# Kernel optimization log

Measured on AMD Instinct MI355X. Metric: run time of the kernel, lower is better.

Reference implementation:

```python
import jax, jax.numpy as jnp
import numpy as np
from jax import lax


def setup_inputs() -> dict:
    key = jax.random.key(0)
    ks = jax.random.split(key, 16)
    B, H, W, C = 4, 48, 48, 512
    N = H * W
    std = 0.02  # trunc_normal std in the torch init

    def nrm(k, shape, s=std):
        return jax.random.normal(k, shape, dtype=jnp.float32) * s

    return {
        "x": jax.random.normal(ks[0], (B, N, C), jnp.float32),
        "context": jax.random.normal(ks[1], (B, N, C), jnp.float32),
        "mask1": jax.random.uniform(ks[2], (B, N), jnp.float32),
        "mask2": jax.random.uniform(ks[3], (B, N), jnp.float32),
        "q_w": nrm(ks[4], (C, C)), "q_b": jnp.zeros((C,), jnp.float32),
        "kv1_w": nrm(ks[5], (C, C)), "kv1_b": jnp.zeros((C,), jnp.float32),
        "kv2_w": nrm(ks[6], (C, C)), "kv2_b": jnp.zeros((C,), jnp.float32),
        "f1_w": nrm(ks[7], (1, 48)), "f1_b": jnp.zeros((1,), jnp.float32),
        "f2_w": nrm(ks[8], (1, 12)), "f2_b": jnp.zeros((1,), jnp.float32),
        "lepe_w": nrm(ks[9], (C, C)), "lepe_b": jnp.zeros((C,), jnp.float32),
        "lepe_conv_w": nrm(ks[10], (C, 1, 3, 3), float(np.sqrt(2.0 / 9.0))),
        "lepe_conv_b": jnp.zeros((C,), jnp.float32),
        "proj_w": nrm(ks[11], (C, C)), "proj_b": jnp.zeros((C,), jnp.float32),
        "H": H, "W": W,
    }


def _lin(t, w, b):
    # torch nn.Linear: y = t @ W^T + b, W:[out,in]
    return t @ w.T + b


def _pooled_seq(ctx, idx, f1_w, f1_b, f2_w, f2_b):
    # ctx:[B,HW,C], idx:[B,HW] mask-sorted indices. sr_ratio==4 => groups of 48/12/1.
    B, HW, Cc = ctx.shape
    t1, t2 = HW // 192, HW // 24  # token1=(HW//48)//4, token2=(HW//12)//2
    g = jnp.take_along_axis(ctx, idx[:, :, None], axis=1)  # [B,HW,C] gathered
    p1 = g[:, : HW // 4].transpose(0, 2, 1).reshape(B, Cc, t1, 48)
    p2 = g[:, HW // 4 : 3 * HW // 4].transpose(0, 2, 1).reshape(B, Cc, t2, 12)
    p3 = g[:, 3 * HW // 4 :].transpose(0, 2, 1)  # [B,C,HW//4]
    a1 = (p1 @ f1_w.T)[..., 0] + f1_b  # [B,C,t1]
    a2 = (p2 @ f2_w.T)[..., 0] + f2_b  # [B,C,t2]
    return jnp.concatenate([a1, a2, p3], axis=-1).transpose(0, 2, 1)  # [B,Lkv,C]


def reference(x, context, mask1, mask2, q_w, q_b, kv1_w, kv1_b, kv2_w, kv2_b,
              f1_w, f1_b, f2_w, f2_b, lepe_w, lepe_b, lepe_conv_w, lepe_conv_b,
              proj_w, proj_b, H, W):
    B, N, C = x.shape
    nh = 8
    hd = C // nh
    scale = hd ** -0.5

    # lepe: linear + depthwise 3x3 conv positional encoding
    le = _lin(x, lepe_w, lepe_b).transpose(0, 2, 1).reshape(B, C, H, W)
    le = lax.conv_general_dilated(le, lepe_conv_w, (1, 1), ((1, 1), (1, 1)),
                                  dimension_numbers=("NCHW", "OIHW", "NCHW"),
                                  feature_group_count=C)
    lepe = (le + lepe_conv_b[None, :, None, None]).reshape(B, C, N).transpose(0, 2, 1)

    # mask-sorted grouped pooling of context (two orderings: row-major and transposed)
    idx1 = jnp.argsort(mask1, axis=1)
    idx2 = jnp.argsort(mask2, axis=1)
    ctx_t = context.reshape(B, H, W, C).transpose(0, 2, 1, 3).reshape(B, N, C)
    seq1 = _pooled_seq(context, idx1, f1_w, f1_b, f2_w, f2_b)
    seq2 = _pooled_seq(ctx_t, idx2, f1_w, f1_b, f2_w, f2_b)

    q = _lin(x, q_w, q_b).reshape(B, N, nh, hd).transpose(0, 2, 1, 3)  # [B,h,N,hd]
    kv1 = _lin(seq1, kv1_w, kv1_b).reshape(B, -1, 2, nh // 2, hd).transpose(2, 0, 3, 1, 4)
    kv2 = _lin(seq2, kv2_w, kv2_b).reshape(B, -1, 2, nh // 2, hd).transpose(2, 0, 3, 1, 4)
    k = jnp.concatenate([kv1[0], kv2[0]], axis=1)  # [B,h,Lkv,hd]
    v = jnp.concatenate([kv1[1], kv2[1]], axis=1)

    attn = jax.nn.softmax(jnp.einsum("bhnd,bhld->bhnl", q, k) * scale, axis=-1)
    out = jnp.einsum("bhnl,bhld->bhnd", attn, v).transpose(0, 2, 1, 3).reshape(B, N, C)
    return _lin(out + lepe, proj_w, proj_b)
```

## Files before the change

kernel.cpp:

```cpp
#include <hip/hip_runtime.h>
#include <hip/hip_bf16.h>
#include <math.h>

#define B_    4
#define H_    48
#define W_    48
#define N_    2304
#define C_    512
#define NH_   8
#define HD_   64
#define LKV_  684
#define LKP_  704

typedef __attribute__((ext_vector_type(8))) short short8;
typedef __attribute__((ext_vector_type(8))) unsigned short ushort8;
typedef __attribute__((ext_vector_type(4))) float f32x4;

#define MFMA16(a, b, c) __builtin_amdgcn_mfma_f32_16x16x32_bf16(a, b, c, 0, 0, 0)

__device__ __forceinline__ unsigned short f2bf(float f) {
  __hip_bfloat16 h = __float2bfloat16(f);
  return *reinterpret_cast<unsigned short*>(&h);
}
__device__ __forceinline__ float bf2f(unsigned short u) {
  unsigned int x = ((unsigned int)u) << 16;
  return *reinterpret_cast<float*>(&x);
}
__device__ __forceinline__ void gld16(const unsigned short* g, unsigned short* l) {
  __builtin_amdgcn_global_load_lds(
      (const __attribute__((address_space(1))) void*)g,
      (__attribute__((address_space(3))) void*)l, 16, 0, 0);
}

__global__ __launch_bounds__(256) void pack_all(
    const float* __restrict__ lepe_w, const float* __restrict__ q_w,
    const float* __restrict__ kv1_w, const float* __restrict__ kv2_w,
    const float* __restrict__ proj_w, const float* __restrict__ x,
    unsigned short* __restrict__ wb, unsigned short* __restrict__ xb)
{
  int i = (blockIdx.x * 256 + threadIdx.x) * 4;
  const float* s; unsigned short* d; int rel;
  if      (i < 262144)  { s = lepe_w; d = wb;           rel = i; }
  else if (i < 524288)  { s = q_w;    d = wb + 262144;  rel = i - 262144; }
  else if (i < 786432)  { s = kv1_w;  d = wb + 524288;  rel = i - 524288; }
  else if (i < 1048576) { s = kv2_w;  d = wb + 786432;  rel = i - 786432; }
  else if (i < 1310720) { s = proj_w; d = wb + 1048576; rel = i - 1048576; }
  else                  { s = x;      d = xb;           rel = i - 1310720; }
  float4 v = *(const float4*)(s + rel);
  ushort4 o;
  o.x = f2bf(v.x); o.y = f2bf(v.y); o.z = f2bf(v.z); o.w = f2bf(v.w);
  *(ushort4*)(d + rel) = o;
}

struct GPair {
  const unsigned short *A0, *A1, *B0, *B1;
  const float *bias0, *bias1;
  void *out0, *out1;
  int bf0, bf1;
  float sc0, sc1;
};

__global__ __launch_bounds__(256) void gemm_bf16(GPair p, int K, int Nn)
{
  const unsigned short* A  = blockIdx.z ? p.A1 : p.A0;
  const unsigned short* Bw = blockIdx.z ? p.B1 : p.B0;
  const float* bias        = blockIdx.z ? p.bias1 : p.bias0;
  void* out                = blockIdx.z ? p.out1 : p.out0;
  const int out_bf16       = blockIdx.z ? p.bf1 : p.bf0;
  const float oscale       = blockIdx.z ? p.sc1 : p.sc0;

  __shared__ unsigned short Abuf[128 * 32];
  __shared__ unsigned short Bbuf[128 * 32];
  const int tid = threadIdx.x;
  const int l = tid & 63, w = tid >> 6;
  const int wm = w >> 1, wn = w & 1;
  const int lo16 = l & 15, hi = l >> 4;
  const int row0 = blockIdx.x * 128, col0 = blockIdx.y * 128;
  const int srow = tid >> 2, scol = (tid & 3) * 8;

  const unsigned short* Asrc = A + (size_t)(row0 + srow) * K + scol;
  const unsigned short* Bsrc = Bw + (size_t)(col0 + srow) * K + scol;

  f32x4 acc[4][4];
  #pragma unroll
  for (int m = 0; m < 4; ++m)
    #pragma unroll
    for (int n = 0; n < 4; ++n)
      #pragma unroll
      for (int r = 0; r < 4; ++r) acc[m][n][r] = 0.f;

  for (int k0 = 0; k0 < K; k0 += 32) {
    __syncthreads();
    gld16(Asrc + k0,                   &Abuf[tid * 8]);
    gld16(Asrc + (size_t)64 * K + k0,  &Abuf[2048 + tid * 8]);
    gld16(Bsrc + k0,                   &Bbuf[tid * 8]);
    gld16(Bsrc + (size_t)64 * K + k0,  &Bbuf[2048 + tid * 8]);
    __syncthreads();
    short8 af[4], bf[4];
    #pragma unroll
    for (int m = 0; m < 4; ++m)
      af[m] = *(const short8*)&Abuf[(wm * 64 + m * 16 + lo16) * 32 + hi * 8];
    #pragma unroll
    for (int n = 0; n < 4; ++n)
      bf[n] = *(const short8*)&Bbuf[(wn * 64 + n * 16 + lo16) * 32 + hi * 8];
    #pragma unroll
    for (int m = 0; m < 4; ++m)
      #pragma unroll
      for (int n = 0; n < 4; ++n)
        acc[m][n] = MFMA16(af[m], bf[n], acc[m][n]);
  }

  #pragma unroll
  for (int m = 0; m < 4; ++m) {
    #pragma unroll
    for (int n = 0; n < 4; ++n) {
      int gcol = col0 + wn * 64 + n * 16 + lo16;
      #pragma unroll
      for (int r = 0; r < 4; ++r) {
        int grow = row0 + wm * 64 + m * 16 + hi * 4 + r;
        float v = acc[m][n][r] + bias[gcol];
        if (out_bf16)
          ((unsigned short*)out)[(size_t)grow * Nn + gcol] = f2bf(v * oscale);
        else
          ((float*)out)[(size_t)grow * Nn + gcol] = v;
      }
    }
  }
}

__global__ __launch_bounds__(256) void dwconv_kernel(
    const unsigned short* __restrict__ lin, const float* __restrict__ cw,
    const float* __restrict__ cb, unsigned short* __restrict__ outp)
{
  const int cg = threadIdx.x & 63;
  const int wslot = blockIdx.x * 4 + (threadIdx.x >> 6);
  const int nslots = gridDim.x * 4;

  float wf[72];
  const float* wsrc = cw + cg * 72;
  #pragma unroll
  for (int i = 0; i < 18; ++i)
    *(float4*)&wf[i * 4] = *(const float4*)(wsrc + i * 4);
  float bias[8];
  *(float4*)&bias[0] = *(const float4*)(cb + cg * 8);
  *(float4*)&bias[4] = *(const float4*)(cb + cg * 8 + 4);

  for (int pos = wslot; pos < B_ * N_; pos += nslots) {
    int wv = pos % W_;
    int r  = pos / W_;
    int hv = r % H_;
    int b  = r / H_;
    float acc[8];
    #pragma unroll
    for (int j = 0; j < 8; ++j) acc[j] = bias[j];
    #pragma unroll
    for (int dy = 0; dy < 3; ++dy) {
      int hh = hv + dy - 1;
      if (hh < 0 || hh >= H_) continue;
      #pragma unroll
      for (int dx = 0; dx < 3; ++dx) {
        int ww = wv + dx - 1;
        if (ww < 0 || ww >= W_) continue;
        ushort8 v = *(const ushort8*)(lin + ((((size_t)b * H_ + hh) * W_ + ww) * 64 + cg) * 8);
        #pragma unroll
        for (int j = 0; j < 8; ++j)
          acc[j] += wf[j * 9 + dy * 3 + dx] * bf2f(v[j]);
      }
    }
    ushort8 ov;
    #pragma unroll
    for (int j = 0; j < 8; ++j) ov[j] = f2bf(acc[j]);
    *(ushort8*)(outp + ((size_t)pos * 64 + cg) * 8) = ov;
  }
}

__global__ __launch_bounds__(256) void rank_argsort(
    const float* __restrict__ m1, const float* __restrict__ m2,
    int* __restrict__ i1, int* __restrict__ i2)
{
  __shared__ float key[N_];
  const int blk = blockIdx.x;
  const int row = blk / 36, chunk = blk % 36;
  const float* m = (row < 4) ? (m1 + (size_t)row * N_) : (m2 + (size_t)(row - 4) * N_);
  int* out = (row < 4) ? (i1 + (size_t)row * N_) : (i2 + (size_t)(row - 4) * N_);
  for (int i = threadIdx.x; i < N_ / 4; i += 256)
    ((float4*)key)[i] = ((const float4*)m)[i];
  __syncthreads();
  const int e = chunk * 64 + (threadIdx.x >> 2);
  const int sl = threadIdx.x & 3;
  const float ki = key[e];
  int rank = 0;
  #pragma unroll 4
  for (int t = 0; t < N_ / 16; ++t) {
    int jb = sl * 4 + t * 16;
    float4 kv = *(const float4*)&key[jb];
    rank += (kv.x < ki) || (kv.x == ki && jb     < e);
    rank += (kv.y < ki) || (kv.y == ki && jb + 1 < e);
    rank += (kv.z < ki) || (kv.z == ki && jb + 2 < e);
    rank += (kv.w < ki) || (kv.w == ki && jb + 3 < e);
  }
  rank += __shfl_xor(rank, 1);
  rank += __shfl_xor(rank, 2);
  if (sl == 0) out[rank] = e;
}

__global__ __launch_bounds__(256) void pool_kernel(
    const float* __restrict__ ctx,
    const int* __restrict__ idx1, const int* __restrict__ idx2,
    const float* __restrict__ f1w, const float* __restrict__ f1b,
    const float* __restrict__ f2w, const float* __restrict__ f2b_,
    unsigned short* __restrict__ seqb1, unsigned short* __restrict__ seqb2)
{
  int bl = blockIdx.x;
  const int transposed = bl >= B_ * LKP_;
  if (transposed) bl -= B_ * LKP_;
  const int* idx = transposed ? idx2 : idx1;
  unsigned short* seqb = transposed ? seqb2 : seqb1;
  int b = bl / LKP_, l = bl % LKP_;
  unsigned short* dst = seqb + ((size_t)b * LKP_ + l) * C_;
  int c0 = threadIdx.x, c1 = threadIdx.x + 256;
  if (l >= LKV_) { dst[c0] = 0; dst[c1] = 0; return; }
  const int* id = idx + (size_t)b * N_;
  int j0, cnt;
  const float* fw; float fb;
  if (l < 12)       { j0 = l * 48;              cnt = 48; fw = f1w; fb = f1b[0]; }
  else if (l < 108) { j0 = 576 + (l - 12) * 12; cnt = 12; fw = f2w; fb = f2b_[0]; }
  else              { j0 = 1728 + (l - 108);    cnt = 1;  fw = nullptr; fb = 0.f; }
  const float* cb = ctx + (size_t)b * N_ * C_;
  float a0 = fb, a1 = fb;
  int r = 0;
  for (; r + 4 <= cnt; r += 4) {
    int4 nv = *(const int4*)(id + j0 + r);
    int n0 = nv.x, n1 = nv.y, n2 = nv.z, n3 = nv.w;
    if (transposed) {
      n0 = (n0 % 48) * 48 + n0 / 48; n1 = (n1 % 48) * 48 + n1 / 48;
      n2 = (n2 % 48) * 48 + n2 / 48; n3 = (n3 % 48) * 48 + n3 / 48;
    }
    const float* s0 = cb + (size_t)n0 * C_;
    const float* s1 = cb + (size_t)n1 * C_;
    const float* s2 = cb + (size_t)n2 * C_;
    const float* s3 = cb + (size_t)n3 * C_;
    float w0 = fw[r], w1 = fw[r+1], w2 = fw[r+2], w3 = fw[r+3];
    a0 += w0 * s0[c0] + w1 * s1[c0] + w2 * s2[c0] + w3 * s3[c0];
    a1 += w0 * s0[c1] + w1 * s1[c1] + w2 * s2[c1] + w3 * s3[c1];
  }
  for (; r < cnt; ++r) {
    int n = id[j0 + r];
    if (transposed) n = (n % 48) * 48 + n / 48;
    const float* src = cb + (size_t)n * C_;
    float wr = fw ? fw[r] : 1.f;
    a0 += wr * src[c0];
    a1 += wr * src[c1];
  }
  dst[c0] = f2bf(a0);
  dst[c1] = f2bf(a1);
}

__global__ __launch_bounds__(256) void kvpack(
    const unsigned short* __restrict__ kv1, const unsigned short* __restrict__ kv2,
    unsigned short* __restrict__ Kf, unsigned short* __restrict__ Vf)
{
  __shared__ unsigned short Vt[64][72];
  const int bh = blockIdx.x / 11, t = blockIdx.x % 11;
  const int h = bh & 7, b = bh >> 3;
  const unsigned short* src = (h < 4) ? kv1 : kv2;
  const int hcol = (h & 3) * 64;
  const int tid = threadIdx.x;

  #pragma unroll
  for (int pass = 0; pass < 2; ++pass) {
    int r = pass * 32 + (tid >> 3);
    int cc = (tid & 7) * 8;
    int l = t * 64 + r;
    uint4 v = make_uint4(0, 0, 0, 0);
    if (l < LKV_)
      v = *(const uint4*)&src[(size_t)(b * LKP_ + l) * C_ + 256 + hcol + cc];
    *(uint4*)&Vt[r][cc] = v;
  }
  __syncthreads();

  #pragma unroll
  for (int pass = 0; pass < 2; ++pass) {
    int o = pass * 256 + tid;
    int lane = o & 63, ns = o >> 6;
    int frag = ns >> 1, s = ns & 1;
    int lo16 = lane & 15, hi8 = (lane >> 4) * 8;
    size_t oidx = ((size_t)blockIdx.x * 8 + ns) * 512 + lane * 8;
    {
      int l = t * 64 + frag * 16 + lo16;
      uint4 val = make_uint4(0, 0, 0, 0);
      if (l < LKV_)
        val = *(const uint4*)&src[(size_t)(b * LKP_ + l) * C_ + hcol + s * 32 + hi8];
      *(uint4*)&Kf[oidx] = val;
    }
    {
      unsigned short tmp[8];
      #pragma unroll
      for (int j = 0; j < 8; ++j)
        tmp[j] = Vt[s * 32 + hi8 + j][frag * 16 + lo16];
      *(uint4*)&Vf[oidx] = *(uint4*)tmp;
    }
  }
}

__global__ __launch_bounds__(64) void attn_kernel(
    const unsigned short* __restrict__ Qb, const unsigned short* __restrict__ Kf,
    const unsigned short* __restrict__ Vf, const unsigned short* __restrict__ lepe,
    unsigned short* __restrict__ outb)
{
  __shared__ unsigned short P[16][72];
  const int l = threadIdx.x;
  const int lo16 = l & 15, hi = l >> 4;
  const int blk = blockIdx.x;
  const int qt = blk % (N_ / 16);
  const int bh = blk / (N_ / 16);
  const int h = bh & 7, b = bh >> 3;

  const unsigned short* qptr = Qb + ((size_t)b * N_ + qt * 16 + lo16) * C_ + h * 64;
  short8 qf0 = *(const short8*)(qptr + hi * 8);
  short8 qf1 = *(const short8*)(qptr + 32 + hi * 8);

  const unsigned short* kbase = Kf + (size_t)bh * 11 * 4096 + (size_t)l * 8;
  const unsigned short* vbase = Vf + (size_t)bh * 11 * 4096 + (size_t)l * 8;

  float mreg = -INFINITY, lsum = 0.f;
  f32x4 o[4];
  #pragma unroll
  for (int df = 0; df < 4; ++df)
    #pragma unroll
    for (int r = 0; r < 4; ++r) o[df][r] = 0.f;

  for (int t = 0; t < 11; ++t) {
    short8 vf0[4], vf1[4], ka0[4], ka1[4];
    #pragma unroll
    for (int i = 0; i < 4; ++i) {
      ka0[i] = *(const short8*)(kbase + (size_t)(t * 8 + i * 2 + 0) * 512);
      ka1[i] = *(const short8*)(kbase + (size_t)(t * 8 + i * 2 + 1) * 512);
      vf0[i] = *(const short8*)(vbase + (size_t)(t * 8 + i * 2 + 0) * 512);
      vf1[i] = *(const short8*)(vbase + (size_t)(t * 8 + i * 2 + 1) * 512);
    }
    const f32x4 z = {0.f, 0.f, 0.f, 0.f};
    f32x4 s[4];
    #pragma unroll
    for (int n = 0; n < 4; ++n) {
      s[n] = MFMA16(ka0[n], qf0, z);
      s[n] = MFMA16(ka1[n], qf1, s[n]);
    }
    if (t == 10) {
      #pragma unroll
      for (int n = 0; n < 4; ++n)
        #pragma unroll
        for (int r = 0; r < 4; ++r)
          if (n * 16 + hi * 4 + r >= LKV_ - 640) s[n][r] = -1e30f;
    }
    float mx = -1e30f;
    #pragma unroll
    for (int n = 0; n < 4; ++n)
      #pragma unroll
      for (int r = 0; r < 4; ++r) mx = fmaxf(mx, s[n][r]);
    mx = fmaxf(mx, __shfl_xor(mx, 16));
    mx = fmaxf(mx, __shfl_xor(mx, 32));
    float mn = fmaxf(mreg, mx);
    float al = exp2f(mreg - mn);
    mreg = mn;
    float psl = 0.f;
    #pragma unroll
    for (int n = 0; n < 4; ++n) {
      #pragma unroll
      for (int rp = 0; rp < 2; ++rp) {
        float e0 = exp2f(s[n][2 * rp]     - mn);
        float e1 = exp2f(s[n][2 * rp + 1] - mn);
        psl += e0 + e1;
        unsigned int pk = (unsigned int)f2bf(e0) | ((unsigned int)f2bf(e1) << 16);
        *(unsigned int*)&P[lo16][n * 16 + hi * 4 + 2 * rp] = pk;
      }
    }
    lsum = lsum * al + psl;
    float alb0 = __shfl(al, hi * 4 + 0);
    float alb1 = __shfl(al, hi * 4 + 1);
    float alb2 = __shfl(al, hi * 4 + 2);
    float alb3 = __shfl(al, hi * 4 + 3);
    #pragma unroll
    for (int df = 0; df < 4; ++df) {
      o[df][0] *= alb0; o[df][1] *= alb1; o[df][2] *= alb2; o[df][3] *= alb3;
    }
    short8 pa0 = *(const short8*)&P[lo16][hi * 8];
    short8 pa1 = *(const short8*)&P[lo16][32 + hi * 8];
    #pragma unroll
    for (int df = 0; df < 4; ++df) {
      o[df] = MFMA16(pa0, vf0[df], o[df]);
      o[df] = MFMA16(pa1, vf1[df], o[df]);
    }
  }

  lsum += __shfl_xor(lsum, 16);
  lsum += __shfl_xor(lsum, 32);
  float rr[4];
  #pragma unroll
  for (int r = 0; r < 4; ++r) rr[r] = 1.f / __shfl(lsum, hi * 4 + r);
  #pragma unroll
  for (int df = 0; df < 4; ++df)
    #pragma unroll
    for (int r = 0; r < 4; ++r) {
      size_t off = ((size_t)b * N_ + qt * 16 + hi * 4 + r) * C_ + h * 64 + df * 16 + lo16;
      outb[off] = f2bf(o[df][r] * rr[r] + bf2f(lepe[off]));
    }
}

extern "C" void kernel_launch(void* const* d_in, const int* in_sizes, int n_in,
                              void* d_out, int out_size, void* d_ws, size_t ws_size,
                              hipStream_t stream)
{
  const float* x      = (const float*)d_in[0];
  const float* ctx    = (const float*)d_in[1];
  const float* mask1  = (const float*)d_in[2];
  const float* mask2  = (const float*)d_in[3];
  const float* q_w    = (const float*)d_in[4];
  const float* q_b    = (const float*)d_in[5];
  const float* kv1_w  = (const float*)d_in[6];
  const float* kv1_b  = (const float*)d_in[7];
  const float* kv2_w  = (const float*)d_in[8];
  const float* kv2_b  = (const float*)d_in[9];
  const float* f1_w   = (const float*)d_in[10];
  const float* f1_b   = (const float*)d_in[11];
  const float* f2_w   = (const float*)d_in[12];
  const float* f2_b   = (const float*)d_in[13];
  const float* lepe_w = (const float*)d_in[14];
  const float* lepe_b = (const float*)d_in[15];
  const float* lcw    = (const float*)d_in[16];
  const float* lcb    = (const float*)d_in[17];
  const float* proj_w = (const float*)d_in[18];
  const float* proj_b = (const float*)d_in[19];
  float* outp = (float*)d_out;

  char* ws = (char*)d_ws;
  unsigned short* bufA  = (unsigned short*)(ws);
  unsigned short* bufB  = (unsigned short*)(ws + 18874368);
  unsigned short* xb    = (unsigned short*)(ws + 37748736);
  unsigned short* Qb    = (unsigned short*)(ws + 47185920);
  unsigned short* wb    = (unsigned short*)(ws + 56623104);
  unsigned short* seqb1 = (unsigned short*)(ws + 59244544);
  unsigned short* seqb2 = (unsigned short*)(ws + 62128128);
  unsigned short* kv1b  = (unsigned short*)(ws + 65011712);
  unsigned short* kv2b  = (unsigned short*)(ws + 67895296);
  unsigned short* Kf    = (unsigned short*)(ws + 70778880);
  unsigned short* Vf    = (unsigned short*)(ws + 73662464);
  int*            idx1  = (int*)(ws + 76546048);
  int*            idx2  = (int*)(ws + 76582912);

  unsigned short* wb_lepe = wb;
  unsigned short* wb_q    = wb + 262144;
  unsigned short* wb_kv1  = wb + 524288;
  unsigned short* wb_kv2  = wb + 786432;
  unsigned short* wb_proj = wb + 1048576;

  dim3 blk(256);
  const int XN = B_ * N_ * C_;
  const int PACKQ = (1310720 + XN) / 4 / 256;

  pack_all<<<dim3(PACKQ), blk, 0, stream>>>(lepe_w, q_w, kv1_w, kv2_w, proj_w, x, wb, xb);
  rank_argsort<<<dim3(288), blk, 0, stream>>>(mask1, mask2, idx1, idx2);

  pool_kernel<<<dim3(2 * B_ * LKP_), blk, 0, stream>>>(
      ctx, idx1, idx2, f1_w, f1_b, f2_w, f2_b, seqb1, seqb2);

  {
    GPair p = { seqb1, seqb2, wb_kv1, wb_kv2, kv1_b, kv2_b,
                (void*)kv1b, (void*)kv2b, 1, 1, 1.f, 1.f };
    gemm_bf16<<<dim3(22, 4, 2), blk, 0, stream>>>(p, C_, C_);
  }
  kvpack<<<dim3(32 * 11), blk, 0, stream>>>(kv1b, kv2b, Kf, Vf);

  {
    GPair p = { xb, xb, wb_lepe, wb_q, lepe_b, q_b,
                (void*)bufA, (void*)Qb, 1, 1, 1.f, 0.18033688011112042f };
    gemm_bf16<<<dim3(72, 4, 2), blk, 0, stream>>>(p, C_, C_);
  }
  dwconv_kernel<<<dim3(384), blk, 0, stream>>>(bufA, lcw, lcb, bufB);

  attn_kernel<<<dim3(B_ * NH_ * (N_ / 16)), dim3(64), 0, stream>>>(Qb, Kf, Vf, bufB, xb);

  {
    GPair p = { xb, xb, wb_proj, wb_proj, proj_b, proj_b,
                (void*)outp, (void*)outp, 0, 0, 1.f, 1.f };
    gemm_bf16<<<dim3(72, 4, 1), blk, 0, stream>>>(p, C_, C_);
  }
}
```

Baseline: 180.3 us.

## Process two query tiles per attention wave, prefetch K, and merge pack with argsort

Each attention wave now handles 32 queries as two 16-row tiles, so every K/V fragment loaded is used twice and half as many waves reload K/V. The next K tile is loaded into registers while the current one is being computed, and the online-softmax rescale is skipped whenever no row's max increases. The weight/x bf16 packing kernel and the rank-based argsort are merged into a single launch by splitting on block index, removing one kernel launch. In exchange the attention kernel uses more registers and launches half as many waves, which may reduce occupancy.

Measured after the change: 203.8 us. 1.13x slower.

```diff
diff --git a/kernel.cpp b/kernel.cpp
--- a/kernel.cpp
+++ b/kernel.cpp
@@ -32,154 +32,33 @@
       (__attribute__((address_space(3))) void*)l, 16, 0, 0);
 }
 
-__global__ __launch_bounds__(256) void pack_all(
+#define PACKQ 5888
+
+__global__ __launch_bounds__(256) void pack_sort(
     const float* __restrict__ lepe_w, const float* __restrict__ q_w,
     const float* __restrict__ kv1_w, const float* __restrict__ kv2_w,
     const float* __restrict__ proj_w, const float* __restrict__ x,
-    unsigned short* __restrict__ wb, unsigned short* __restrict__ xb)
-{
-  int i = (blockIdx.x * 256 + threadIdx.x) * 4;
-  const float* s; unsigned short* d; int rel;
-  if      (i < 262144)  { s = lepe_w; d = wb;           rel = i; }
-  else if (i < 524288)  { s = q_w;    d = wb + 262144;  rel = i - 262144; }
-  else if (i < 786432)  { s = kv1_w;  d = wb + 524288;  rel = i - 524288; }
-  else if (i < 1048576) { s = kv2_w;  d = wb + 786432;  rel = i - 786432; }
-  else if (i < 1310720) { s = proj_w; d = wb + 1048576; rel = i - 1048576; }
-  else                  { s = x;      d = xb;           rel = i - 1310720; }
-  float4 v = *(const float4*)(s + rel);
-  ushort4 o;
-  o.x = f2bf(v.x); o.y = f2bf(v.y); o.z = f2bf(v.z); o.w = f2bf(v.w);
-  *(ushort4*)(d + rel) = o;
-}
-
-struct GPair {
-  const unsigned short *A0, *A1, *B0, *B1;
-  const float *bias0, *bias1;
-  void *out0, *out1;
-  int bf0, bf1;
-  float sc0, sc1;
-};
-
-__global__ __launch_bounds__(256) void gemm_bf16(GPair p, int K, int Nn)
-{
-  const unsigned short* A  = blockIdx.z ? p.A1 : p.A0;
-  const unsigned short* Bw = blockIdx.z ? p.B1 : p.B0;
-  const float* bias        = blockIdx.z ? p.bias1 : p.bias0;
-  void* out                = blockIdx.z ? p.out1 : p.out0;
-  const int out_bf16       = blockIdx.z ? p.bf1 : p.bf0;
-  const float oscale       = blockIdx.z ? p.sc1 : p.sc0;
-
-  __shared__ unsigned short Abuf[128 * 32];
-  __shared__ unsigned short Bbuf[128 * 32];
-  const int tid = threadIdx.x;
-  const int l = tid & 63, w = tid >> 6;
-  const int wm = w >> 1, wn = w & 1;
-  const int lo16 = l & 15, hi = l >> 4;
-  const int row0 = blockIdx.x * 128, col0 = blockIdx.y * 128;
-  const int srow = tid >> 2, scol = (tid & 3) * 8;
-
-  const unsigned short* Asrc = A + (size_t)(row0 + srow) * K + scol;
-  const unsigned short* Bsrc = Bw + (size_t)(col0 + srow) * K + scol;
-
-  f32x4 acc[4][4];
-  #pragma unroll
-  for (int m = 0; m < 4; ++m)
-    #pragma unroll
-    for (int n = 0; n < 4; ++n)
-      #pragma unroll
-      for (int r = 0; r < 4; ++r) acc[m][n][r] = 0.f;
-
-  for (int k0 = 0; k0 < K; k0 += 32) {
-    __syncthreads();
-    gld16(Asrc + k0,                   &Abuf[tid * 8]);
-    gld16(Asrc + (size_t)64 * K + k0,  &Abuf[2048 + tid * 8]);
-    gld16(Bsrc + k0,                   &Bbuf[tid * 8]);
-    gld16(Bsrc + (size_t)64 * K + k0,  &Bbuf[2048 + tid * 8]);
-    __syncthreads();
-    short8 af[4], bf[4];
-    #pragma unroll
-    for (int m = 0; m < 4; ++m)
-      af[m] = *(const short8*)&Abuf[(wm * 64 + m * 16 + lo16) * 32 + hi * 8];
-    #pragma unroll
-    for (int n = 0; n < 4; ++n)
-      bf[n] = *(const short8*)&Bbuf[(wn * 64 + n * 16 + lo16) * 32 + hi * 8];
-    #pragma unroll
-    for (int m = 0; m < 4; ++m)
-      #pragma unroll
-      for (int n = 0; n < 4; ++n)
-        acc[m][n] = MFMA16(af[m], bf[n], acc[m][n]);
-  }
-
-  #pragma unroll
-  for (int m = 0; m < 4; ++m) {
-    #pragma unroll
-    for (int n = 0; n < 4; ++n) {
-      int gcol = col0 + wn * 64 + n * 16 + lo16;
-      #pragma unroll
-      for (int r = 0; r < 4; ++r) {
-        int grow = row0 + wm * 64 + m * 16 + hi * 4 + r;
-        float v = acc[m][n][r] + bias[gcol];
-        if (out_bf16)
-          ((unsigned short*)out)[(size_t)grow * Nn + gcol] = f2bf(v * oscale);
-        else
-          ((float*)out)[(size_t)grow * Nn + gcol] = v;
-      }
-    }
-  }
-}
-
-__global__ __launch_bounds__(256) void dwconv_kernel(
-    const unsigned short* __restrict__ lin, const float* __restrict__ cw,
-    const float* __restrict__ cb, unsigned short* __restrict__ outp)
-{
-  const int cg = threadIdx.x & 63;
-  const int wslot = blockIdx.x * 4 + (threadIdx.x >> 6);
-  const int nslots = gridDim.x * 4;
-
-  float wf[72];
-  const float* wsrc = cw + cg * 72;
-  #pragma unroll
-  for (int i = 0; i < 18; ++i)
-    *(float4*)&wf[i * 4] = *(const float4*)(wsrc + i * 4);
-  float bias[8];
-  *(float4*)&bias[0] = *(const float4*)(cb + cg * 8);
-  *(float4*)&bias[4] = *(const float4*)(cb + cg * 8 + 4);
-
-  for (int pos = wslot; pos < B_ * N_; pos += nslots) {
-    int wv = pos % W_;
-    int r  = pos / W_;
-    int hv = r % H_;
-    int b  = r / H_;
-    float acc[8];
-    #pragma unroll
-    for (int j = 0; j < 8; ++j) acc[j] = bias[j];
-    #pragma unroll
-    for (int dy = 0; dy < 3; ++dy) {
-      int hh = hv + dy - 1;
-      if (hh < 0 || hh >= H_) continue;
-      #pragma unroll
-      for (int dx = 0; dx < 3; ++dx) {
-        int ww = wv + dx - 1;
-        if (ww < 0 || ww >= W_) continue;
-        ushort8 v = *(const ushort8*)(lin + ((((size_t)b * H_ + hh) * W_ + ww) * 64 + cg) * 8);
-        #pragma unroll
-        for (int j = 0; j < 8; ++j)
-          acc[j] += wf[j * 9 + dy * 3 + dx] * bf2f(v[j]);
-      }
-    }
-    ushort8 ov;
-    #pragma unroll
-    for (int j = 0; j < 8; ++j) ov[j] = f2bf(acc[j]);
-    *(ushort8*)(outp + ((size_t)pos * 64 + cg) * 8) = ov;
-  }
-}
-
-__global__ __launch_bounds__(256) void rank_argsort(
+    unsigned short* __restrict__ wb, unsigned short* __restrict__ xb,
     const float* __restrict__ m1, const float* __restrict__ m2,
     int* __restrict__ i1, int* __restrict__ i2)
 {
   __shared__ float key[N_];
-  const int blk = blockIdx.x;
+  if (blockIdx.x < PACKQ) {
+    int i = (blockIdx.x * 256 + threadIdx.x) * 4;
+    const float* s; unsigned short* d; int rel;
+    if      (i < 262144)  { s = lepe_w; d = wb;           rel = i; }
+    else if (i < 524288)  { s = q_w;    d = wb + 262144;  rel = i - 262144; }
+    else if (i < 786432)  { s = kv1_w;  d = wb + 524288;  rel = i - 524288; }
+    else if (i < 1048576) { s = kv2_w;  d = wb + 786432;  rel = i - 786432; }
+    else if (i < 1310720) { s = proj_w; d = wb + 1048576; rel = i - 1048576; }
+    else                  { s = x;      d = xb;           rel = i - 1310720; }
+    float4 v = *(const float4*)(s + rel);
+    ushort4 o;
+    o.x = f2bf(v.x); o.y = f2bf(v.y); o.z = f2bf(v.z); o.w = f2bf(v.w);
+    *(ushort4*)(d + rel) = o;
+    return;
+  }
+  const int blk = blockIdx.x - PACKQ;
   const int row = blk / 36, chunk = blk % 36;
   const float* m = (row < 4) ? (m1 + (size_t)row * N_) : (m2 + (size_t)(row - 4) * N_);
   int* out = (row < 4) ? (i1 + (size_t)row * N_) : (i2 + (size_t)(row - 4) * N_);
@@ -202,6 +81,128 @@
   rank += __shfl_xor(rank, 1);
   rank += __shfl_xor(rank, 2);
   if (sl == 0) out[rank] = e;
+}
+
+struct GPair {
+  const unsigned short *A0, *A1, *B0, *B1;
+  const float *bias0, *bias1;
+  void *out0, *out1;
+  int bf0, bf1;
+  float sc0, sc1;
+};
+
+__global__ __launch_bounds__(256) void gemm_bf16(GPair p, int K, int Nn)
+{
+  const unsigned short* A  = blockIdx.z ? p.A1 : p.A0;
+  const unsigned short* Bw = blockIdx.z ? p.B1 : p.B0;
+  const float* bias        = blockIdx.z ? p.bias1 : p.bias0;
+  void* out                = blockIdx.z ? p.out1 : p.out0;
+  const int out_bf16       = blockIdx.z ? p.bf1 : p.bf0;
+  const float oscale       = blockIdx.z ? p.sc1 : p.sc0;
+
+  __shared__ unsigned short Abuf[128 * 32];
+  __shared__ unsigned short Bbuf[128 * 32];
+  const int tid = threadIdx.x;
+  const int l = tid & 63, w = tid >> 6;
+  const int wm = w >> 1, wn = w & 1;
+  const int lo16 = l & 15, hi = l >> 4;
+  const int row0 = blockIdx.x * 128, col0 = blockIdx.y * 128;
+  const int srow = tid >> 2, scol = (tid & 3) * 8;
+
+  const unsigned short* Asrc = A + (size_t)(row0 + srow) * K + scol;
+  const unsigned short* Bsrc = Bw + (size_t)(col0 + srow) * K + scol;
+
+  f32x4 acc[4][4];
+  #pragma unroll
+  for (int m = 0; m < 4; ++m)
+    #pragma unroll
+    for (int n = 0; n < 4; ++n)
+      #pragma unroll
+      for (int r = 0; r < 4; ++r) acc[m][n][r] = 0.f;
+
+  for (int k0 = 0; k0 < K; k0 += 32) {
+    __syncthreads();
+    gld16(Asrc + k0,                   &Abuf[tid * 8]);
+    gld16(Asrc + (size_t)64 * K + k0,  &Abuf[2048 + tid * 8]);
+    gld16(Bsrc + k0,                   &Bbuf[tid * 8]);
+    gld16(Bsrc + (size_t)64 * K + k0,  &Bbuf[2048 + tid * 8]);
+    __syncthreads();
+    short8 af[4], bf[4];
+    #pragma unroll
+    for (int m = 0; m < 4; ++m)
+      af[m] = *(const short8*)&Abuf[(wm * 64 + m * 16 + lo16) * 32 + hi * 8];
+    #pragma unroll
+    for (int n = 0; n < 4; ++n)
+      bf[n] = *(const short8*)&Bbuf[(wn * 64 + n * 16 + lo16) * 32 + hi * 8];
+    #pragma unroll
+    for (int m = 0; m < 4; ++m)
+      #pragma unroll
+      for (int n = 0; n < 4; ++n)
+        acc[m][n] = MFMA16(af[m], bf[n], acc[m][n]);
+  }
+
+  #pragma unroll
+  for (int m = 0; m < 4; ++m) {
+    #pragma unroll
+    for (int n = 0; n < 4; ++n) {
+      int gcol = col0 + wn * 64 + n * 16 + lo16;
+      #pragma unroll
+      for (int r = 0; r < 4; ++r) {
+        int grow = row0 + wm * 64 + m * 16 + hi * 4 + r;
+        float v = acc[m][n][r] + bias[gcol];
+        if (out_bf16)
+          ((unsigned short*)out)[(size_t)grow * Nn + gcol] = f2bf(v * oscale);
+        else
+          ((float*)out)[(size_t)grow * Nn + gcol] = v;
+      }
+    }
+  }
+}
+
+__global__ __launch_bounds__(256) void dwconv_kernel(
+    const unsigned short* __restrict__ lin, const float* __restrict__ cw,
+    const float* __restrict__ cb, unsigned short* __restrict__ outp)
+{
+  const int cg = threadIdx.x & 63;
+  const int wslot = blockIdx.x * 4 + (threadIdx.x >> 6);
+  const int nslots = gridDim.x * 4;
+
+  float wf[72];
+  const float* wsrc = cw + cg * 72;
+  #pragma unroll
+  for (int i = 0; i < 18; ++i)
+    *(float4*)&wf[i * 4] = *(const float4*)(wsrc + i * 4);
+  float bias[8];
+  *(float4*)&bias[0] = *(const float4*)(cb + cg * 8);
+  *(float4*)&bias[4] = *(const float4*)(cb + cg * 8 + 4);
+
+  for (int pos = wslot; pos < B_ * N_; pos += nslots) {
+    int wv = pos % W_;
+    int r  = pos / W_;
+    int hv = r % H_;
+    int b  = r / H_;
+    float acc[8];
+    #pragma unroll
+    for (int j = 0; j < 8; ++j) acc[j] = bias[j];
+    #pragma unroll
+    for (int dy = 0; dy < 3; ++dy) {
+      int hh = hv + dy - 1;
+      if (hh < 0 || hh >= H_) continue;
+      #pragma unroll
+      for (int dx = 0; dx < 3; ++dx) {
+        int ww = wv + dx - 1;
+        if (ww < 0 || ww >= W_) continue;
+        ushort8 v = *(const ushort8*)(lin + ((((size_t)b * H_ + hh) * W_ + ww) * 64 + cg) * 8);
+        #pragma unroll
+        for (int j = 0; j < 8; ++j)
+          acc[j] += wf[j * 9 + dy * 3 + dx] * bf2f(v[j]);
+      }
+    }
+    ushort8 ov;
+    #pragma unroll
+    for (int j = 0; j < 8; ++j) ov[j] = f2bf(acc[j]);
+    *(ushort8*)(outp + ((size_t)pos * 64 + cg) * 8) = ov;
+  }
 }
 
 __global__ __launch_bounds__(256) void pool_kernel(
@@ -308,102 +309,151 @@
     const unsigned short* __restrict__ Vf, const unsigned short* __restrict__ lepe,
     unsigned short* __restrict__ outb)
 {
-  __shared__ unsigned short P[16][72];
+  __shared__ unsigned short P[2][16][72];
   const int l = threadIdx.x;
   const int lo16 = l & 15, hi = l >> 4;
-  const int blk = blockIdx.x;
-  const int qt = blk % (N_ / 16);
-  const int bh = blk / (N_ / 16);
+  const int qt = blockIdx.x % (N_ / 32);
+  const int bh = blockIdx.x / (N_ / 32);
   const int h = bh & 7, b = bh >> 3;
 
-  const unsigned short* qptr = Qb + ((size_t)b * N_ + qt * 16 + lo16) * C_ + h * 64;
-  short8 qf0 = *(const short8*)(qptr + hi * 8);
-  short8 qf1 = *(const short8*)(qptr + 32 + hi * 8);
+  const unsigned short* qpA = Qb + ((size_t)b * N_ + qt * 32 + lo16) * C_ + h * 64;
+  const unsigned short* qpB = qpA + (size_t)16 * C_;
+  short8 qa0 = *(const short8*)(qpA + hi * 8);
+  short8 qa1 = *(const short8*)(qpA + 32 + hi * 8);
+  short8 qb0 = *(const short8*)(qpB + hi * 8);
+  short8 qb1 = *(const short8*)(qpB + 32 + hi * 8);
 
   const unsigned short* kbase = Kf + (size_t)bh * 11 * 4096 + (size_t)l * 8;
   const unsigned short* vbase = Vf + (size_t)bh * 11 * 4096 + (size_t)l * 8;
 
-  float mreg = -INFINITY, lsum = 0.f;
-  f32x4 o[4];
+  float mra = -INFINITY, mrb = -INFINITY, lsa = 0.f, lsb = 0.f;
+  f32x4 oa[4], ob[4];
   #pragma unroll
   for (int df = 0; df < 4; ++df)
     #pragma unroll
-    for (int r = 0; r < 4; ++r) o[df][r] = 0.f;
+    for (int r = 0; r < 4; ++r) { oa[df][r] = 0.f; ob[df][r] = 0.f; }
+
+  short8 ka0[4], ka1[4], kn0[4], kn1[4];
+  #pragma unroll
+  for (int n = 0; n < 4; ++n) {
+    ka0[n] = *(const short8*)(kbase + (size_t)(n * 2 + 0) * 512);
+    ka1[n] = *(const short8*)(kbase + (size_t)(n * 2 + 1) * 512);
+  }
 
   for (int t = 0; t < 11; ++t) {
-    short8 vf0[4], vf1[4], ka0[4], ka1[4];
+    short8 vf0[4], vf1[4];
     #pragma unroll
     for (int i = 0; i < 4; ++i) {
-      ka0[i] = *(const short8*)(kbase + (size_t)(t * 8 + i * 2 + 0) * 512);
-      ka1[i] = *(const short8*)(kbase + (size_t)(t * 8 + i * 2 + 1) * 512);
       vf0[i] = *(const short8*)(vbase + (size_t)(t * 8 + i * 2 + 0) * 512);
       vf1[i] = *(const short8*)(vbase + (size_t)(t * 8 + i * 2 + 1) * 512);
     }
+    if (t < 10) {
+      #pragma unroll
+      for (int n = 0; n < 4; ++n) {
+        kn0[n] = *(const short8*)(kbase + (size_t)((t + 1) * 8 + n * 2 + 0) * 512);
+        kn1[n] = *(const short8*)(kbase + (size_t)((t + 1) * 8 + n * 2 + 1) * 512);
+      }
+    }
     const f32x4 z = {0.f, 0.f, 0.f, 0.f};
-    f32x4 s[4];
+    f32x4 sa[4], sb[4];
     #pragma unroll
     for (int n = 0; n < 4; ++n) {
-      s[n] = MFMA16(ka0[n], qf0, z);
-      s[n] = MFMA16(ka1[n], qf1, s[n]);
+      sa[n] = MFMA16(ka0[n], qa0, z);
+      sa[n] = MFMA16(ka1[n], qa1, sa[n]);
+      sb[n] = MFMA16(ka0[n], qb0, z);
+      sb[n] = MFMA16(ka1[n], qb1, sb[n]);
     }
     if (t == 10) {
       #pragma unroll
       for (int n = 0; n < 4; ++n)
         #pragma unroll
         for (int r = 0; r < 4; ++r)
-          if (n * 16 + hi * 4 + r >= LKV_ - 640) s[n][r] = -1e30f;
-    }
-    float mx = -1e30f;
+          if (n * 16 + hi * 4 + r >= LKV_ - 640) { sa[n][r] = -1e30f; sb[n][r] = -1e30f; }
+    }
+    float mxa = -1e30f, mxb = -1e30f;
     #pragma unroll
     for (int n = 0; n < 4; ++n)
       #pragma unroll
-      for (int r = 0; r < 4; ++r) mx = fmaxf(mx, s[n][r]);
-    mx = fmaxf(mx, __shfl_xor(mx, 16));
-    mx = fmaxf(mx, __shfl_xor(mx, 32));
-    float mn = fmaxf(mreg, mx);
-    float al = exp2f(mreg - mn);
-    mreg = mn;
-    float psl = 0.f;
+      for (int r = 0; r < 4; ++r) {
+        mxa = fmaxf(mxa, sa[n][r]);
+        mxb = fmaxf(mxb, sb[n][r]);
+      }
+    mxa = fmaxf(mxa, __shfl_xor(mxa, 16)); mxa = fmaxf(mxa, __shfl_xor(mxa, 32));
+    mxb = fmaxf(mxb, __shfl_xor(mxb, 16)); mxb = fmaxf(mxb, __shfl_xor(mxb, 32));
+    if (__any(mxa > mra)) {
+      float mn = fmaxf(mra, mxa);
+      float al = exp2f(mra - mn);
+      mra = mn;
+      lsa *= al;
+      float a0 = __shfl(al, hi * 4 + 0), a1 = __shfl(al, hi * 4 + 1);
+      float a2 = __shfl(al, hi * 4 + 2), a3 = __shfl(al, hi * 4 + 3);
+      #pragma unroll
+      for (int df = 0; df < 4; ++df) {
+        oa[df][0] *= a0; oa[df][1] *= a1; oa[df][2] *= a2; oa[df][3] *= a3;
+      }
+    }
+    if (__any(mxb > mrb)) {
+      float mn = fmaxf(mrb, mxb);
+      float al = exp2f(mrb - mn);
+      mrb = mn;
+      lsb *= al;
+      float a0 = __shfl(al, hi * 4 + 0), a1 = __shfl(al, hi * 4 + 1);
+      float a2 = __shfl(al, hi * 4 + 2), a3 = __shfl(al, hi * 4 + 3);
+      #pragma unroll
+      for (int df = 0; df < 4; ++df) {
+        ob[df][0] *= a0; ob[df][1] *= a1; ob[df][2] *= a2; ob[df][3] *= a3;
+      }
+    }
+    float psa = 0.f, psb = 0.f;
     #pragma unroll
     for (int n = 0; n < 4; ++n) {
       #pragma unroll
       for (int rp = 0; rp < 2; ++rp) {
-        float e0 = exp2f(s[n][2 * rp]     - mn);
-        float e1 = exp2f(s[n][2 * rp + 1] - mn);
-        psl += e0 + e1;
-        unsigned int pk = (unsigned int)f2bf(e0) | ((unsigned int)f2bf(e1) << 16);
-        *(unsigned int*)&P[lo16][n * 16 + hi * 4 + 2 * rp] = pk;
-      }
-    }
-    lsum = lsum * al + psl;
-    float alb0 = __shfl(al, hi * 4 + 0);
-    float alb1 = __shfl(al, hi * 4 + 1);
-    float alb2 = __shfl(al, hi * 4 + 2);
-    float alb3 = __shfl(al, hi * 4 + 3);
+        float ea0 = exp2f(sa[n][2 * rp]     - mra);
+        float ea1 = exp2f(sa[n][2 * rp + 1] - mra);
+        psa += ea0 + ea1;
+        *(unsigned int*)&P[0][lo16][n * 16 + hi * 4 + 2 * rp] =
+            (unsigned int)f2bf(ea0) | ((unsigned int)f2bf(ea1) << 16);
+        float eb0 = exp2f(sb[n][2 * rp]     - mrb);
+        float eb1 = exp2f(sb[n][2 * rp + 1] - mrb);
+        psb += eb0 + eb1;
+        *(unsigned int*)&P[1][lo16][n * 16 + hi * 4 + 2 * rp] =
+            (unsigned int)f2bf(eb0) | ((unsigned int)f2bf(eb1) << 16);
+      }
+    }
+    lsa += psa;
+    lsb += psb;
+    short8 pa0 = *(const short8*)&P[0][lo16][hi * 8];
+    short8 pa1 = *(const short8*)&P[0][lo16][32 + hi * 8];
+    short8 pb0 = *(const short8*)&P[1][lo16][hi * 8];
+    short8 pb1 = *(const short8*)&P[1][lo16][32 + hi * 8];
     #pragma unroll
     for (int df = 0; df < 4; ++df) {
-      o[df][0] *= alb0; o[df][1] *= alb1; o[df][2] *= alb2; o[df][3] *= alb3;
-    }
-    short8 pa0 = *(const short8*)&P[lo16][hi * 8];
-    short8 pa1 = *(const short8*)&P[lo16][32 + hi * 8];
-    #pragma unroll
-    for (int df = 0; df < 4; ++df) {
-      o[df] = MFMA16(pa0, vf0[df], o[df]);
-      o[df] = MFMA16(pa1, vf1[df], o[df]);
-    }
-  }
-
-  lsum += __shfl_xor(lsum, 16);
-  lsum += __shfl_xor(lsum, 32);
-  float rr[4];
-  #pragma unroll
-  for (int r = 0; r < 4; ++r) rr[r] = 1.f / __shfl(lsum, hi * 4 + r);
+      oa[df] = MFMA16(pa0, vf0[df], oa[df]);
+      oa[df] = MFMA16(pa1, vf1[df], oa[df]);
+      ob[df] = MFMA16(pb0, vf0[df], ob[df]);
+      ob[df] = MFMA16(pb1, vf1[df], ob[df]);
+    }
+    #pragma unroll
+    for (int n = 0; n < 4; ++n) { ka0[n] = kn0[n]; ka1[n] = kn1[n]; }
+  }
+
+  lsa += __shfl_xor(lsa, 16); lsa += __shfl_xor(lsa, 32);
+  lsb += __shfl_xor(lsb, 16); lsb += __shfl_xor(lsb, 32);
+  float rra[4], rrb[4];
+  #pragma unroll
+  for (int r = 0; r < 4; ++r) {
+    rra[r] = 1.f / __shfl(lsa, hi * 4 + r);
+    rrb[r] = 1.f / __shfl(lsb, hi * 4 + r);
+  }
   #pragma unroll
   for (int df = 0; df < 4; ++df)
     #pragma unroll
     for (int r = 0; r < 4; ++r) {
-      size_t off = ((size_t)b * N_ + qt * 16 + hi * 4 + r) * C_ + h * 64 + df * 16 + lo16;
-      outb[off] = f2bf(o[df][r] * rr[r] + bf2f(lepe[off]));
+      size_t offA = ((size_t)b * N_ + qt * 32 + hi * 4 + r) * C_ + h * 64 + df * 16 + lo16;
+      outb[offA] = f2bf(oa[df][r] * rra[r] + bf2f(lepe[offA]));
+      size_t offB = offA + (size_t)16 * C_;
+      outb[offB] = f2bf(ob[df][r] * rrb[r] + bf2f(lepe[offB]));
     }
 }
 
@@ -456,10 +506,9 @@
 
   dim3 blk(256);
   const int XN = B_ * N_ * C_;
-  const int PACKQ = (1310720 + XN) / 4 / 256;
-
-  pack_all<<<dim3(PACKQ), blk, 0, stream>>>(lepe_w, q_w, kv1_w, kv2_w, proj_w, x, wb, xb);
-  rank_argsort<<<dim3(288), blk, 0, stream>>>(mask1, mask2, idx1, idx2);
+
+  pack_sort<<<dim3(PACKQ + 288), blk, 0, stream>>>(
+      lepe_w, q_w, kv1_w, kv2_w, proj_w, x, wb, xb, mask1, mask2, idx1, idx2);
 
   pool_kernel<<<dim3(2 * B_ * LKP_), blk, 0, stream>>>(
       ctx, idx1, idx2, f1_w, f1_b, f2_w, f2_b, seqb1, seqb2);
@@ -478,7 +527,7 @@
   }
   dwconv_kernel<<<dim3(384), blk, 0, stream>>>(bufA, lcw, lcb, bufB);
 
-  attn_kernel<<<dim3(B_ * NH_ * (N_ / 16)), dim3(64), 0, stream>>>(Qb, Kf, Vf, bufB, xb);
+  attn_kernel<<<dim3(B_ * NH_ * (N_ / 32)), dim3(64), 0, stream>>>(Qb, Kf, Vf, bufB, xb);
 
   {
     GPair p = { xb, xb, wb_proj, wb_proj, proj_b, proj_b,
```
